# Performance work log

Measured on AMD Instinct MI355X. Metric: run time of the kernel, lower is better.

Reference implementation:

```python
import jax, jax.numpy as jnp
import numpy as np

B, S, E, H, D = 2, 2048, 1024, 16, 64  # batch, seq(=max_seq_len), embed_dim, heads, atten_dim


def setup_inputs() -> dict:
    key = jax.random.key(0)
    ks = jax.random.split(key, 9)
    s = 0.02
    return {
        "x": jax.random.normal(ks[0], (B, S, E), jnp.float32),
        "Wq": jax.random.normal(ks[1], (H, E, D), jnp.float32) * s,
        "Wk": jax.random.normal(ks[2], (H, E, D), jnp.float32) * s,
        "Wv": jax.random.normal(ks[3], (H, E, D), jnp.float32) * s,
        "bq": jax.random.normal(ks[4], (H, D), jnp.float32) * s,
        "bk": jax.random.normal(ks[5], (H, D), jnp.float32) * s,
        "bv": jax.random.normal(ks[6], (H, D), jnp.float32) * s,
        "Wp": jax.random.normal(ks[7], (H * D, E), jnp.float32) * s,
        "bp": jax.random.normal(ks[8], (E,), jnp.float32) * s,
    }


def reference(x, Wq, Wk, Wv, bq, bk, bv, Wp, bp):
    scale = jnp.sqrt(jnp.float32(D))
    # per-head projections, all heads at once: [B,H,S,D]
    q = jnp.einsum("bse,hed->bhsd", x, Wq) + bq[:, None, :]
    k = jnp.einsum("bse,hed->bhsd", x, Wk) + bk[:, None, :]
    v = jnp.einsum("bse,hed->bhsd", x, Wv) + bv[:, None, :]
    # causal scores [B,H,S,S], additive -inf mask above diagonal (as in the buffer)
    score = jnp.einsum("bhsd,bhtd->bhst", q, k) / scale
    mask = jnp.triu(jnp.full((S, S), -jnp.inf, jnp.float32), k=1)
    score = score + mask
    probs = jax.nn.softmax(score, axis=-1)
    attn = jnp.einsum("bhst,bhtd->bhsd", probs, v)
    # concat heads -> [B,S,H*D], then projection + ReLU
    concat = attn.transpose(0, 2, 1, 3).reshape(B, S, H * D)
    out = jax.nn.relu(concat @ Wp + bp)
    return out
```

## Files before the change

kernel.cpp:

```cpp
#include <hip/hip_runtime.h>

#define S_LEN 2048
#define E_DIM 1024
#define H_NUM 16
#define D_DIM 64

typedef unsigned short u16;
using bf16x8 = __attribute__((ext_vector_type(8))) short;
using f32x4  = __attribute__((ext_vector_type(4))) float;
using f32x16 = __attribute__((ext_vector_type(16))) float;

#define MFMA16(A, B, C) __builtin_amdgcn_mfma_f32_16x16x32_bf16(A, B, C, 0, 0, 0)
#define MFMA32(A, B, C) __builtin_amdgcn_mfma_f32_32x32x16_bf16(A, B, C, 0, 0, 0)
#define QSCALE 0.18033688011112042f

__device__ __forceinline__ u16 f2bf(float f) {
    unsigned u = __float_as_uint(f);
    u += 0x7fffu + ((u >> 16) & 1u);
    return (u16)(u >> 16);
}
__device__ __forceinline__ f32x4 fzero4() { f32x4 z; z[0]=0.f; z[1]=0.f; z[2]=0.f; z[3]=0.f; return z; }
__device__ __forceinline__ f32x16 fzero16() {
    f32x16 z;
    #pragma unroll
    for (int i = 0; i < 16; i++) z[i] = 0.f;
    return z;
}

__device__ __forceinline__ unsigned cvtpk(float a, float b) {
    unsigned r;
    asm("v_cvt_pk_bf16_f32 %0, %1, %2" : "=v"(r) : "v"(a), "v"(b));
    return r;
}
__device__ __forceinline__ float fexp2(float x) {
#if __has_builtin(__builtin_amdgcn_exp2f)
    return __builtin_amdgcn_exp2f(x);
#else
    float r; asm("v_exp_f32 %0, %1" : "=v"(r) : "v"(x)); return r;
#endif
}
__device__ __forceinline__ float frcp(float x) {
#if __has_builtin(__builtin_amdgcn_rcpf)
    return __builtin_amdgcn_rcpf(x);
#else
    float r; asm("v_rcp_f32 %0, %1" : "=v"(r) : "v"(x)); return r;
#endif
}

__device__ __forceinline__ void gll16(const u16* g, u16* l) {
    __builtin_amdgcn_global_load_lds(
        (const __attribute__((address_space(1))) void*)g,
        (__attribute__((address_space(3))) void*)l, 16, 0, 0);
}

__device__ __forceinline__ void stage64(const u16* __restrict__ g, int gstride,
                                        u16* l, int wave, int lane) {
    #pragma unroll
    for (int i = 0; i < 2; i++) {
        const int r  = wave * 16 + i * 8 + (lane >> 3);
        const int sl = (lane & 7) ^ (r & 7);
        gll16(g + (size_t)r * gstride + sl * 8, l + (wave * 16 + i * 8) * 64);
    }
}
__device__ __forceinline__ bf16x8 ldswz(const u16* t, int rr, int hh, int quad) {
    const int sl = ((hh << 2) + quad) ^ (rr & 7);
    return *(const bf16x8*)(t + rr * 64 + sl * 8);
}
__device__ __forceinline__ bf16x8 ldfr(const u16* t, int rr, int sl) {
    return *(const bf16x8*)(t + rr * 64 + ((sl ^ (rr & 7)) * 8));
}

__device__ __forceinline__ void cvt_t_tile(const float* __restrict__ bin, u16* __restrict__ bout,
                                           int R, int C, int r0, int c0) {
    __shared__ float t[64][65];
    const int tid = threadIdx.x;
    const int lr = tid >> 2, lc = (tid & 3) * 16;

    const float* src = bin + (size_t)(r0 + lr) * C + c0 + lc;
    #pragma unroll
    for (int j = 0; j < 4; j++) {
        float4 f = *(const float4*)(src + j * 4);
        t[lr][lc + j * 4 + 0] = f.x; t[lr][lc + j * 4 + 1] = f.y;
        t[lr][lc + j * 4 + 2] = f.z; t[lr][lc + j * 4 + 3] = f.w;
    }
    __syncthreads();

    u16* dst = bout + (size_t)(c0 + lr) * R + r0 + lc;
    u16 vals[16];
    #pragma unroll
    for (int i = 0; i < 16; i++) vals[i] = f2bf(t[lc + i][lr]);
    uint4 pa, pb;
    pa.x = vals[0] | (vals[1] << 16);  pa.y = vals[2] | (vals[3] << 16);
    pa.z = vals[4] | (vals[5] << 16);  pa.w = vals[6] | (vals[7] << 16);
    pb.x = vals[8] | (vals[9] << 16);  pb.y = vals[10] | (vals[11] << 16);
    pb.z = vals[12] | (vals[13] << 16); pb.w = vals[14] | (vals[15] << 16);
    *(uint4*)dst = pa;
    *(uint4*)(dst + 8) = pb;
}

__global__ __launch_bounds__(256) void cvt_all(
    const float* __restrict__ x, u16* __restrict__ xb, int n,
    const float* __restrict__ Wq, const float* __restrict__ Wk, const float* __restrict__ Wv,
    u16* __restrict__ wqt, u16* __restrict__ wkt, u16* __restrict__ wvt,
    const float* __restrict__ Wp, u16* __restrict__ wpt)
{
    const int bid = blockIdx.x;
    if (bid < 4096) {
        int i4 = (bid * 256 + threadIdx.x) * 4;
        if (i4 < n) {
            float4 f = *(const float4*)(x + i4);
            unsigned lo = (unsigned)f2bf(f.x) | ((unsigned)f2bf(f.y) << 16);
            unsigned hi = (unsigned)f2bf(f.z) | ((unsigned)f2bf(f.w) << 16);
            uint2 p; p.x = lo; p.y = hi;
            *(uint2*)(xb + i4) = p;
        }
    } else if (bid < 4096 + 768) {
        const int t  = bid - 4096;
        const int z  = t >> 4;
        const int ry = t & 15;
        const int which = z >> 4, bh = z & 15;
        const float* in = (which == 0) ? Wq : (which == 1) ? Wk : Wv;
        u16* outp = (which == 0) ? wqt : (which == 1) ? wkt : wvt;
        cvt_t_tile(in + (size_t)bh * E_DIM * D_DIM, outp + (size_t)bh * E_DIM * D_DIM,
                   E_DIM, D_DIM, ry * 64, 0);
    } else {
        const int t = bid - (4096 + 768);
        cvt_t_tile(Wp, wpt, H_NUM * D_DIM, E_DIM, (t >> 4) * 64, (t & 15) * 64);
    }
}

__global__ __launch_bounds__(128, 2) void qkv_gemm(
    const u16* __restrict__ xb, const u16* __restrict__ wcat,
    const float* __restrict__ bq, const float* __restrict__ bk, const float* __restrict__ bv,
    u16* __restrict__ oq, u16* __restrict__ okk, u16* __restrict__ ov)
{
    const int m0 = blockIdx.x * 128;
    const int n0 = blockIdx.y * 128;

    __shared__ u16 As[2][64 * 64];
    __shared__ u16 Bs[2][64 * 64];

    const int tid  = threadIdx.x;
    const int wave = tid >> 6, lane = tid & 63, quad = lane >> 4, l16 = lane & 15;

    f32x4 acc[8][4];
    #pragma unroll
    for (int j = 0; j < 8; j++)
        #pragma unroll
        for (int mi = 0; mi < 4; mi++) acc[j][mi] = fzero4();

#define STAGE(K0, BUF)                                                               \
    _Pragma("unroll")                                                                \
    for (int i = 0; i < 2; i++) {                                                    \
        const int r  = wave * 32 + i * 8 + (lane >> 3);           \
        const int s  = (lane & 7) ^ (r & 7);                      \
        const int mr = r + ((s >> 2) << 6);                      \
        const int kc = (s & 3) * 8;                              \
        gll16(xb   + (size_t)(m0 + mr) * E_DIM + (K0) + kc,                          \
              &As[BUF][(wave * 32 + i * 8) * 64]);                                   \
        gll16(wcat + (size_t)(n0 + mr) * E_DIM + (K0) + kc,                          \
              &Bs[BUF][(wave * 32 + i * 8) * 64]);                                   \
        const int r2  = wave * 32 + 16 + i * 8 + (lane >> 3);                        \
        const int s2  = (lane & 7) ^ (r2 & 7);                                       \
        const int mr2 = r2 + ((s2 >> 2) << 6);                                       \
        const int kc2 = (s2 & 3) * 8;                                                \
        gll16(xb   + (size_t)(m0 + mr2) * E_DIM + (K0) + kc2,                        \
              &As[BUF][(wave * 32 + 16 + i * 8) * 64]);                              \
        gll16(wcat + (size_t)(n0 + mr2) * E_DIM + (K0) + kc2,                        \
              &Bs[BUF][(wave * 32 + 16 + i * 8) * 64]);                              \
    }

    STAGE(0, 0);

    for (int kt = 0; kt < 32; kt++) {
        __syncthreads();
        if (kt < 31) {
            const int kn = (kt + 1) * 32;
            if ((kt & 1) == 0) { STAGE(kn, 1); } else { STAGE(kn, 0); }
        }
        const u16* Ac = As[kt & 1];
        const u16* Bc = Bs[kt & 1];

        bf16x8 af[4];
        #pragma unroll
        for (int mi = 0; mi < 4; mi++) {
            const int row = mi * 16 + l16;
            af[mi] = *(const bf16x8*)(&Ac[row * 64 + ((((wave << 2) + quad)) ^ (row & 7)) * 8]);
        }
        __builtin_amdgcn_s_setprio(1);
        #pragma unroll
        for (int j = 0; j < 8; j++) {
            const int row = (j & 3) * 16 + l16;
            bf16x8 bfv = *(const bf16x8*)(&Bc[row * 64 +
                              ((((j >> 2) << 2) + quad) ^ (row & 7)) * 8]);
            #pragma unroll
            for (int mi = 0; mi < 4; mi++)
                acc[j][mi] = MFMA16(af[mi], bfv, acc[j][mi]);
        }
        __builtin_amdgcn_s_setprio(0);
    }
#undef STAGE

    const int t = n0 >> 10;
    if (t < 2) {
        const float scl = (t == 0) ? QSCALE : 1.0f;
        const float* bias = (t == 0) ? bq : bk;
        u16* dst = (t == 0) ? oq : okk;
        #pragma unroll
        for (int j = 0; j < 8; j++) {
            const int n = n0 + j * 16 + l16;
            const int h = (n >> 6) & 15, d = n & 63;
            float bia = bias[h * D_DIM + d];
            #pragma unroll
            for (int mi = 0; mi < 4; mi++) {
                #pragma unroll
                for (int r = 0; r < 4; r++) {
                    int m = m0 + wave * 64 + mi * 16 + quad * 4 + r;
                    int b = m >> 11, s = m & 2047;
                    dst[((size_t)(b * H_NUM + h) * S_LEN + s) * D_DIM + d] =
                        f2bf((acc[j][mi][r] + bia) * scl);
                }
            }
        }
    } else {
        const int b  = m0 >> 11, s0 = m0 & 2047;
        const int h0 = (n0 >> 6) & 15;
        u16* Tb0 = &As[0][0];
        u16* Tb1 = &Bs[0][0];
        #pragma unroll
        for (int pass = 0; pass < 2; ++pass) {
            __syncthreads();
            if (wave == pass) {
                #pragma unroll
                for (int j = 0; j < 8; j++) {
                    const int n = n0 + j * 16 + l16;
                    const int d = n & 63, hh = (n >> 6) & 15;
                    const float bia = bv[hh * D_DIM + d];
                    u16* Tb = (j < 4) ? Tb0 : Tb1;
                    const int nl = (j & 3) * 16 + l16;
                    #pragma unroll
                    for (int mi = 0; mi < 4; mi++) {
                        uint2 pk;
                        pk.x = cvtpk(acc[j][mi][0] + bia, acc[j][mi][1] + bia);
                        pk.y = cvtpk(acc[j][mi][2] + bia, acc[j][mi][3] + bia);
                        *(uint2*)(&Tb[nl * 72 + mi * 16 + quad * 4]) = pk;
                    }
                }
            }
            __syncthreads();
            #pragma unroll
            for (int g = 0; g < 8; ++g) {
                const int rowi = g * 16 + (tid >> 3);
                const int ml = (tid & 7) * 8;
                const u16* srcp = (rowi < 64 ? Tb0 : Tb1) + (rowi & 63) * 72 + ml;
                const int hh = h0 + (rowi >> 6), d = rowi & 63;
                u16* dstp = ov + ((size_t)(b * H_NUM + hh) * D_DIM + d) * S_LEN
                               + s0 + pass * 64 + ml;
                *(uint4*)dstp = *(const uint4*)srcp;
            }
        }
    }
}

__global__ __launch_bounds__(256, 2) void attn_fwd(
    const u16* __restrict__ q, const u16* __restrict__ k, const u16* __restrict__ vt,
    u16* __restrict__ concat)
{
    const int bid  = blockIdx.x;
    const int halfg = bid >> 8;
    const int pi   = (bid & 255) >> 5;
    const int p    = halfg ? (15 - pi) : pi;
    const int g    = bid & 31;
    const int hd   = g & 15;
    const int bb   = g >> 4;
    const int qa = p, qb = 31 - p;

    const size_t headoff = (size_t)(bb * H_NUM + hd) * S_LEN * D_DIM;
    const u16* qptr = q  + headoff;
    const u16* kptr = k  + headoff;
    const u16* vptr = vt + headoff;

    __shared__ u16 Ks[2][64 * 64];
    __shared__ u16 Vts[2][64 * 64];
    __shared__ float Ls[4][32];

    const int tid  = threadIdx.x;
    const int wave = tid >> 6, lane = tid & 63;
    const int l32 = lane & 31, hh = lane >> 5;

    const int mytile = (wave >> 1) ? qa : qb;
    const int qhalf  = wave & 1;

    stage64(qptr + (size_t)qb * 64 * D_DIM, D_DIM, Ks[0],  wave, lane);
    stage64(qptr + (size_t)qa * 64 * D_DIM, D_DIM, Vts[0], wave, lane);
    __syncthreads();

    bf16x8 qf[4];
    {
        const u16* Qsrc = (wave >> 1) ? &Vts[0][0] : &Ks[0][0];
        const int row = qhalf * 32 + l32;
        #pragma unroll
        for (int c = 0; c < 4; c++) qf[c] = ldfr(Qsrc, row, c * 2 + hh);
    }
    __syncthreads();

    stage64(kptr, D_DIM, Ks[0],  wave, lane);
    stage64(vptr, S_LEN, Vts[0], wave, lane);

    f32x16 o0 = fzero16(), o1 = fzero16();
    float ls = 0.f;
    const int qg   = mytile * 64 + qhalf * 32 + l32;
    const int kk4h = 4 * hh;

    for (int kt = 0; kt <= qb; kt++) {
        __syncthreads();
        if (kt < qb) {
            stage64(kptr + (size_t)(kt + 1) * 64 * D_DIM, D_DIM, Ks[(kt + 1) & 1],  wave, lane);
            stage64(vptr + (kt + 1) * 64,                 S_LEN, Vts[(kt + 1) & 1], wave, lane);
        }
        if (kt > mytile) continue;

        const u16* Kc = &Ks[kt & 1][0];
        const u16* Vc = &Vts[kt & 1][0];

        f32x16 s0 = fzero16(), s1 = fzero16();
        __builtin_amdgcn_s_setprio(1);
        #pragma unroll
        for (int c = 0; c < 4; c++) {
            bf16x8 ak0 = ldfr(Kc, l32,      c * 2 + hh);
            bf16x8 ak1 = ldfr(Kc, 32 + l32, c * 2 + hh);
            s0 = MFMA32(ak0, qf[c], s0);
            s1 = MFMA32(ak1, qf[c], s1);
        }
        __builtin_amdgcn_s_setprio(0);

        float pe0[16], pe1[16];
        if (kt == mytile) {
            #pragma unroll
            for (int r = 0; r < 16; r++) {
                const int kkg = kt * 64 + (r & 3) + 8 * (r >> 2) + kk4h;
                pe0[r] = (kkg      > qg) ? 0.f : fexp2(s0[r]);
                pe1[r] = (kkg + 32 > qg) ? 0.f : fexp2(s1[r]);
            }
        } else {
            #pragma unroll
            for (int r = 0; r < 16; r++) { pe0[r] = fexp2(s0[r]); pe1[r] = fexp2(s1[r]); }
        }
        #pragma unroll
        for (int r = 0; r < 16; r++) ls += pe0[r] + pe1[r];

        bf16x8 pa[4];
#define BUILD_PA(PE, D0, D1)                                                      \
        {                                                                         \
            unsigned X0 = cvtpk(PE[0], PE[1]),   X1 = cvtpk(PE[2], PE[3]);        \
            unsigned Y0 = cvtpk(PE[4], PE[5]),   Y1 = cvtpk(PE[6], PE[7]);        \
            asm("v_permlane32_swap_b32 %0, %1" : "+v"(X0), "+v"(Y0));             \
            asm("v_permlane32_swap_b32 %0, %1" : "+v"(X1), "+v"(Y1));             \
            int4 f0; f0.x = (int)X0; f0.y = (int)X1; f0.z = (int)Y0; f0.w = (int)Y1; \
            D0 = *(bf16x8*)&f0;                                                   \
            unsigned Z0 = cvtpk(PE[8], PE[9]),   Z1 = cvtpk(PE[10], PE[11]);      \
            unsigned W0 = cvtpk(PE[12], PE[13]), W1 = cvtpk(PE[14], PE[15]);      \
            asm("v_permlane32_swap_b32 %0, %1" : "+v"(Z0), "+v"(W0));             \
            asm("v_permlane32_swap_b32 %0, %1" : "+v"(Z1), "+v"(W1));             \
            int4 f1; f1.x = (int)Z0; f1.y = (int)Z1; f1.z = (int)W0; f1.w = (int)W1; \
            D1 = *(bf16x8*)&f1;                                                   \
        }
        BUILD_PA(pe0, pa[0], pa[1]);
        BUILD_PA(pe1, pa[2], pa[3]);
#undef BUILD_PA

        __builtin_amdgcn_s_setprio(1);
        #pragma unroll
        for (int j = 0; j < 4; j++) {
            bf16x8 bv0 = ldfr(Vc, l32,      j * 2 + hh);
            bf16x8 bv1 = ldfr(Vc, 32 + l32, j * 2 + hh);
            o0 = MFMA32(pa[j], bv0, o0);
            o1 = MFMA32(pa[j], bv1, o1);
        }
        __builtin_amdgcn_s_setprio(0);
    }

    ls += __shfl_xor(ls, 32);
    if (hh == 0) Ls[wave][l32] = ls;

    #pragma unroll
    for (int r = 0; r < 16; r++) {
        const int qlr = (r & 3) + 8 * (r >> 2) + kk4h;
        const float li = frcp(Ls[wave][qlr]);
        const int qrow = mytile * 64 + qhalf * 32 + qlr;
        u16* dst = concat + ((size_t)(bb * S_LEN + qrow)) * E_DIM + hd * D_DIM;
        dst[l32]      = f2bf(o0[r] * li);
        dst[32 + l32] = f2bf(o1[r] * li);
    }
}

__global__ __launch_bounds__(256, 2) void out_proj(
    const u16* __restrict__ concat, const u16* __restrict__ wpt,
    const float* __restrict__ bp, float* __restrict__ out)
{
    const int bid = blockIdx.x;
    const int mt  = (bid & 7) * 8 + ((bid >> 3) & 7);
    const int nt0 = bid >> 6;
    const int m0 = mt * 64;
    const int n0 = nt0 * 128;

    __shared__ u16 As[2][64 * 64];
    __shared__ u16 Bs[2][128 * 64];

    const int tid  = threadIdx.x;
    const int wave = tid >> 6, lane = tid & 63, quad = lane >> 4, l16 = lane & 15;
    const int mh = wave >> 1, nh = wave & 1;

    f32x4 acc[4][2];
    #pragma unroll
    for (int j = 0; j < 4; j++)
        #pragma unroll
        for (int mi = 0; mi < 2; mi++) acc[j][mi] = fzero4();

    stage64(concat + (size_t)m0 * E_DIM, E_DIM, As[0], wave, lane);
    stage64(wpt + (size_t)n0 * E_DIM,        E_DIM, Bs[0],           wave, lane);
    stage64(wpt + (size_t)(n0 + 64) * E_DIM, E_DIM, Bs[0] + 64 * 64, wave, lane);

    for (int kt = 0; kt < 16; kt++) {
        __syncthreads();
        if (kt < 15) {
            const int k0 = (kt + 1) * 64;
            u16* an = As[(kt + 1) & 1];
            u16* bn = Bs[(kt + 1) & 1];
            stage64(concat + (size_t)m0 * E_DIM + k0, E_DIM, an, wave, lane);
            stage64(wpt + (size_t)n0 * E_DIM + k0,        E_DIM, bn,           wave, lane);
            stage64(wpt + (size_t)(n0 + 64) * E_DIM + k0, E_DIM, bn + 64 * 64, wave, lane);
        }
        const u16* Ac = As[kt & 1];
        const u16* Bc = Bs[kt & 1];

        #pragma unroll
        for (int kq = 0; kq < 2; kq++) {
            bf16x8 af[2];
            #pragma unroll
            for (int mi = 0; mi < 2; mi++)
                af[mi] = ldswz(Ac, mh * 32 + mi * 16 + l16, kq, quad);
            __builtin_amdgcn_s_setprio(1);
            #pragma unroll
            for (int j = 0; j < 4; j++) {
                bf16x8 bfv = ldswz(Bc, nh * 64 + j * 16 + l16, kq, quad);
                #pragma unroll
                for (int mi = 0; mi < 2; mi++)
                    acc[j][mi] = MFMA16(af[mi], bfv, acc[j][mi]);
            }
            __builtin_amdgcn_s_setprio(0);
        }
    }

    #pragma unroll
    for (int j = 0; j < 4; j++) {
        int n = n0 + nh * 64 + j * 16 + l16;
        float bia = bp[n];
        #pragma unroll
        for (int mi = 0; mi < 2; mi++) {
            #pragma unroll
            for (int r = 0; r < 4; r++) {
                int m = m0 + mh * 32 + mi * 16 + quad * 4 + r;
                out[(size_t)m * E_DIM + n] = fmaxf(acc[j][mi][r] + bia, 0.f);
            }
        }
    }
}

extern "C" void kernel_launch(void* const* d_in, const int* in_sizes, int n_in,
                              void* d_out, int out_size, void* d_ws, size_t ws_size,
                              hipStream_t stream)
{
    (void)in_sizes; (void)n_in; (void)out_size; (void)ws_size;
    const float* x  = (const float*)d_in[0];
    const float* Wq = (const float*)d_in[1];
    const float* Wk = (const float*)d_in[2];
    const float* Wv = (const float*)d_in[3];
    const float* bq = (const float*)d_in[4];
    const float* bk = (const float*)d_in[5];
    const float* bv = (const float*)d_in[6];
    const float* Wp = (const float*)d_in[7];
    const float* bp = (const float*)d_in[8];
    float* out = (float*)d_out;

    const size_t QKV_ELEMS = (size_t)2 * H_NUM * S_LEN * D_DIM;
    const size_t W_ELEMS   = (size_t)H_NUM * E_DIM * D_DIM;

    u16* q   = (u16*)d_ws;
    u16* k   = q   + QKV_ELEMS;
    u16* v   = k   + QKV_ELEMS;
    u16* cc  = v   + QKV_ELEMS;
    u16* xb  = cc  + QKV_ELEMS;
    u16* wqt = xb  + QKV_ELEMS;
    u16* wkt = wqt + W_ELEMS;
    u16* wvt = wkt + W_ELEMS;
    u16* wpt = wvt + W_ELEMS;

    cvt_all<<<dim3(4096 + 768 + 256), 256, 0, stream>>>(
        x, xb, (int)QKV_ELEMS, Wq, Wk, Wv, wqt, wkt, wvt, Wp, wpt);

    qkv_gemm<<<dim3(32, 24), 128, 0, stream>>>(xb, wqt, bq, bk, bv, q, k, v);
    attn_fwd<<<dim3(512), 256, 0, stream>>>(q, k, v, cc);
    out_proj<<<dim3(512), 256, 0, stream>>>(cc, wpt, bp, out);
}
```

Baseline: 178.5 us.

## Split attention work across waves by key half instead of query tile

Previously waves 0-1 handled query tile qb and waves 2-3 handled qa, so the qa waves sat idle for iterations after qa while the qb waves kept working. Now each wave covers 32 keys of every key tile for both query tiles, and the two key-half partial outputs and row sums are combined through shared memory at the end. The goal is to balance MFMA work across all four waves each iteration, at the cost of extra accumulator registers and a cross-wave reduction in LDS.

```diff
diff --git a/kernel.cpp b/kernel.cpp
--- a/kernel.cpp
+++ b/kernel.cpp
@@ -282,74 +282,39 @@
 
     __shared__ u16 Ks[2][64 * 64];
     __shared__ u16 Vts[2][64 * 64];
-    __shared__ float Ls[4][32];
+    __shared__ float Lsb[2][2][32];
+    __shared__ float Lsa[2][2][32];
 
     const int tid  = threadIdx.x;
     const int wave = tid >> 6, lane = tid & 63;
     const int l32 = lane & 31, hh = lane >> 5;
-
-    const int mytile = (wave >> 1) ? qa : qb;
-    const int qhalf  = wave & 1;
+    const int qhalf = wave & 1, kh = wave >> 1;
 
     stage64(qptr + (size_t)qb * 64 * D_DIM, D_DIM, Ks[0],  wave, lane);
     stage64(qptr + (size_t)qa * 64 * D_DIM, D_DIM, Vts[0], wave, lane);
     __syncthreads();
 
-    bf16x8 qf[4];
+    bf16x8 qfb[4], qfa[4];
     {
-        const u16* Qsrc = (wave >> 1) ? &Vts[0][0] : &Ks[0][0];
         const int row = qhalf * 32 + l32;
         #pragma unroll
-        for (int c = 0; c < 4; c++) qf[c] = ldfr(Qsrc, row, c * 2 + hh);
+        for (int c = 0; c < 4; c++) {
+            qfb[c] = ldfr(&Ks[0][0],  row, c * 2 + hh);
+            qfa[c] = ldfr(&Vts[0][0], row, c * 2 + hh);
+        }
     }
     __syncthreads();
 
     stage64(kptr, D_DIM, Ks[0],  wave, lane);
     stage64(vptr, S_LEN, Vts[0], wave, lane);
 
-    f32x16 o0 = fzero16(), o1 = fzero16();
-    float ls = 0.f;
-    const int qg   = mytile * 64 + qhalf * 32 + l32;
-    const int kk4h = 4 * hh;
-
-    for (int kt = 0; kt <= qb; kt++) {
-        __syncthreads();
-        if (kt < qb) {
-            stage64(kptr + (size_t)(kt + 1) * 64 * D_DIM, D_DIM, Ks[(kt + 1) & 1],  wave, lane);
-            stage64(vptr + (kt + 1) * 64,                 S_LEN, Vts[(kt + 1) & 1], wave, lane);
-        }
-        if (kt > mytile) continue;
-
-        const u16* Kc = &Ks[kt & 1][0];
-        const u16* Vc = &Vts[kt & 1][0];
-
-        f32x16 s0 = fzero16(), s1 = fzero16();
-        __builtin_amdgcn_s_setprio(1);
-        #pragma unroll
-        for (int c = 0; c < 4; c++) {
-            bf16x8 ak0 = ldfr(Kc, l32,      c * 2 + hh);
-            bf16x8 ak1 = ldfr(Kc, 32 + l32, c * 2 + hh);
-            s0 = MFMA32(ak0, qf[c], s0);
-            s1 = MFMA32(ak1, qf[c], s1);
-        }
-        __builtin_amdgcn_s_setprio(0);
-
-        float pe0[16], pe1[16];
-        if (kt == mytile) {
-            #pragma unroll
-            for (int r = 0; r < 16; r++) {
-                const int kkg = kt * 64 + (r & 3) + 8 * (r >> 2) + kk4h;
-                pe0[r] = (kkg      > qg) ? 0.f : fexp2(s0[r]);
-                pe1[r] = (kkg + 32 > qg) ? 0.f : fexp2(s1[r]);
-            }
-        } else {
-            #pragma unroll
-            for (int r = 0; r < 16; r++) { pe0[r] = fexp2(s0[r]); pe1[r] = fexp2(s1[r]); }
-        }
-        #pragma unroll
-        for (int r = 0; r < 16; r++) ls += pe0[r] + pe1[r];
-
-        bf16x8 pa[4];
+    f32x16 ob0 = fzero16(), ob1 = fzero16();
+    f32x16 oa0 = fzero16(), oa1 = fzero16();
+    float lsb = 0.f, lsa = 0.f;
+    const int qgb = qb * 64 + qhalf * 32 + l32;
+    const int qga = qa * 64 + qhalf * 32 + l32;
+    const int kkbase = kh * 32 + 4 * hh;
+
 #define BUILD_PA(PE, D0, D1)                                                      \
         {                                                                         \
             unsigned X0 = cvtpk(PE[0], PE[1]),   X1 = cvtpk(PE[2], PE[3]);        \
@@ -365,32 +330,143 @@
             int4 f1; f1.x = (int)Z0; f1.y = (int)Z1; f1.z = (int)W0; f1.w = (int)W1; \
             D1 = *(bf16x8*)&f1;                                                   \
         }
-        BUILD_PA(pe0, pa[0], pa[1]);
-        BUILD_PA(pe1, pa[2], pa[3]);
+
+    for (int kt = 0; kt <= qb; kt++) {
+        __syncthreads();
+        if (kt < qb) {
+            stage64(kptr + (size_t)(kt + 1) * 64 * D_DIM, D_DIM, Ks[(kt + 1) & 1],  wave, lane);
+            stage64(vptr + (kt + 1) * 64,                 S_LEN, Vts[(kt + 1) & 1], wave, lane);
+        }
+        const u16* Kc = &Ks[kt & 1][0];
+        const u16* Vc = &Vts[kt & 1][0];
+
+        {
+            f32x16 s = fzero16();
+            __builtin_amdgcn_s_setprio(1);
+            #pragma unroll
+            for (int c = 0; c < 4; c++) {
+                bf16x8 ak = ldfr(Kc, kh * 32 + l32, c * 2 + hh);
+                s = MFMA32(ak, qfb[c], s);
+            }
+            __builtin_amdgcn_s_setprio(0);
+
+            float pe[16];
+            if (kt == qb) {
+                #pragma unroll
+                for (int r = 0; r < 16; r++) {
+                    const int kkg = kt * 64 + kkbase + (r & 3) + 8 * (r >> 2);
+                    pe[r] = (kkg > qgb) ? 0.f : fexp2(s[r]);
+                }
+            } else {
+                #pragma unroll
+                for (int r = 0; r < 16; r++) pe[r] = fexp2(s[r]);
+            }
+            #pragma unroll
+            for (int r = 0; r < 16; r++) lsb += pe[r];
+
+            bf16x8 pa0, pa1;
+            BUILD_PA(pe, pa0, pa1);
+
+            __builtin_amdgcn_s_setprio(1);
+            {
+                bf16x8 v00 = ldfr(Vc, l32,      (2 * kh    ) * 2 + hh);
+                bf16x8 v10 = ldfr(Vc, 32 + l32, (2 * kh    ) * 2 + hh);
+                bf16x8 v01 = ldfr(Vc, l32,      (2 * kh + 1) * 2 + hh);
+                bf16x8 v11 = ldfr(Vc, 32 + l32, (2 * kh + 1) * 2 + hh);
+                ob0 = MFMA32(pa0, v00, ob0);
+                ob1 = MFMA32(pa0, v10, ob1);
+                ob0 = MFMA32(pa1, v01, ob0);
+                ob1 = MFMA32(pa1, v11, ob1);
+            }
+            __builtin_amdgcn_s_setprio(0);
+        }
+
+        if (kt <= qa) {
+            f32x16 s = fzero16();
+            __builtin_amdgcn_s_setprio(1);
+            #pragma unroll
+            for (int c = 0; c < 4; c++) {
+                bf16x8 ak = ldfr(Kc, kh * 32 + l32, c * 2 + hh);
+                s = MFMA32(ak, qfa[c], s);
+            }
+            __builtin_amdgcn_s_setprio(0);
+
+            float pe[16];
+            if (kt == qa) {
+                #pragma unroll
+                for (int r = 0; r < 16; r++) {
+                    const int kkg = kt * 64 + kkbase + (r & 3) + 8 * (r >> 2);
+                    pe[r] = (kkg > qga) ? 0.f : fexp2(s[r]);
+                }
+            } else {
+                #pragma unroll
+                for (int r = 0; r < 16; r++) pe[r] = fexp2(s[r]);
+            }
+            #pragma unroll
+            for (int r = 0; r < 16; r++) lsa += pe[r];
+
+            bf16x8 pa0, pa1;
+            BUILD_PA(pe, pa0, pa1);
+
+            __builtin_amdgcn_s_setprio(1);
+            {
+                bf16x8 v00 = ldfr(Vc, l32,      (2 * kh    ) * 2 + hh);
+                bf16x8 v10 = ldfr(Vc, 32 + l32, (2 * kh    ) * 2 + hh);
+                bf16x8 v01 = ldfr(Vc, l32,      (2 * kh + 1) * 2 + hh);
+                bf16x8 v11 = ldfr(Vc, 32 + l32, (2 * kh + 1) * 2 + hh);
+                oa0 = MFMA32(pa0, v00, oa0);
+                oa1 = MFMA32(pa0, v10, oa1);
+                oa0 = MFMA32(pa1, v01, oa0);
+                oa1 = MFMA32(pa1, v11, oa1);
+            }
+            __builtin_amdgcn_s_setprio(0);
+        }
+    }
 #undef BUILD_PA
 
-        __builtin_amdgcn_s_setprio(1);
-        #pragma unroll
-        for (int j = 0; j < 4; j++) {
-            bf16x8 bv0 = ldfr(Vc, l32,      j * 2 + hh);
-            bf16x8 bv1 = ldfr(Vc, 32 + l32, j * 2 + hh);
-            o0 = MFMA32(pa[j], bv0, o0);
-            o1 = MFMA32(pa[j], bv1, o1);
-        }
-        __builtin_amdgcn_s_setprio(0);
-    }
-
-    ls += __shfl_xor(ls, 32);
-    if (hh == 0) Ls[wave][l32] = ls;
-
-    #pragma unroll
-    for (int r = 0; r < 16; r++) {
-        const int qlr = (r & 3) + 8 * (r >> 2) + kk4h;
-        const float li = frcp(Ls[wave][qlr]);
-        const int qrow = mytile * 64 + qhalf * 32 + qlr;
-        u16* dst = concat + ((size_t)(bb * S_LEN + qrow)) * E_DIM + hd * D_DIM;
-        dst[l32]      = f2bf(o0[r] * li);
-        dst[32 + l32] = f2bf(o1[r] * li);
+    __syncthreads();
+
+    lsb += __shfl_xor(lsb, 32);
+    lsa += __shfl_xor(lsa, 32);
+    if (hh == 0) {
+        Lsb[kh][qhalf][l32] = lsb;
+        Lsa[kh][qhalf][l32] = lsa;
+    }
+
+    float* Rb = (float*)(&Ks[0][0])  + qhalf * 2048;
+    float* Ra = (float*)(&Vts[0][0]) + qhalf * 2048;
+
+    if (kh == 1) {
+        #pragma unroll
+        for (int r = 0; r < 16; r++) {
+            const int qlr = (r & 3) + 8 * (r >> 2) + 4 * hh;
+            Rb[qlr * 64 + l32]      = ob0[r];
+            Rb[qlr * 64 + 32 + l32] = ob1[r];
+            Ra[qlr * 64 + l32]      = oa0[r];
+            Ra[qlr * 64 + 32 + l32] = oa1[r];
+        }
+    }
+    __syncthreads();
+
+    if (kh == 0) {
+        #pragma unroll
+        for (int r = 0; r < 16; r++) {
+            const int qlr = (r & 3) + 8 * (r >> 2) + 4 * hh;
+            const float lib = frcp(Lsb[0][qhalf][qlr] + Lsb[1][qhalf][qlr]);
+            const float lia = frcp(Lsa[0][qhalf][qlr] + Lsa[1][qhalf][qlr]);
+            const float vb0 = ob0[r] + Rb[qlr * 64 + l32];
+            const float vb1 = ob1[r] + Rb[qlr * 64 + 32 + l32];
+            const float va0 = oa0[r] + Ra[qlr * 64 + l32];
+            const float va1 = oa1[r] + Ra[qlr * 64 + 32 + l32];
+            const int qrb = qb * 64 + qhalf * 32 + qlr;
+            const int qra = qa * 64 + qhalf * 32 + qlr;
+            u16* db = concat + ((size_t)(bb * S_LEN + qrb)) * E_DIM + hd * D_DIM;
+            u16* da = concat + ((size_t)(bb * S_LEN + qra)) * E_DIM + hd * D_DIM;
+            db[l32]      = f2bf(vb0 * lib);
+            db[32 + l32] = f2bf(vb1 * lib);
+            da[l32]      = f2bf(va0 * lia);
+            da[32 + l32] = f2bf(va1 * lia);
+        }
     }
 }
 
```

After: 173.0 us. -3.1%, faster.
